# Kernel tuning notes

Measured on AMD Instinct MI355X. Metric: run time of the kernel, lower is better.

The kernel has to match this reference:

```python
import jax, jax.numpy as jnp
import numpy as np

N_NODES = 2048
N_GRAPHS = 64
N_EDGES = 16384
B = 65536
META = 64
TX = 8
NOISE = 128
IN_DIM = N_NODES + 1 + 32 + TX  # 2089


def setup_inputs() -> dict:
    key = jax.random.key(0)
    ks = jax.random.split(key, 11)
    return {
        "batched_graphs": jax.random.randint(ks[0], (B,), 0, N_GRAPHS),
        "batched_chain": jax.random.normal(ks[1], (B,), dtype=jnp.float32),
        "trigger_data": jax.random.normal(ks[2], (B, META), dtype=jnp.float32),
        "tx_start_time": jax.random.normal(ks[3], (B, TX), dtype=jnp.float32),
        "edges": jax.random.randint(ks[4], (N_GRAPHS, 2, N_EDGES), 0, N_NODES),
        "gcn_w": jax.random.normal(ks[5], (), dtype=jnp.float32),
        "gcn_b": jax.random.normal(ks[6], (), dtype=jnp.float32) * 0.01,
        "trig_W": jax.random.normal(ks[7], (META, 32), dtype=jnp.float32) / np.sqrt(META),
        "trig_b": jnp.zeros((32,), dtype=jnp.float32),
        "emb_W": jax.random.normal(ks[8], (IN_DIM, NOISE), dtype=jnp.float32) / np.sqrt(IN_DIM),
        "emb_b": jnp.zeros((NOISE,), dtype=jnp.float32),
    }


def _gcn_one_graph(edge_index, w, b):
    # GCNConv(1,1) on x = ones(n_nodes,1): add self loops, sym-normalize.
    self_idx = jnp.arange(N_NODES, dtype=edge_index.dtype)
    src = jnp.concatenate([edge_index[0], self_idx])
    dst = jnp.concatenate([edge_index[1], self_idx])
    deg = jax.ops.segment_sum(jnp.ones(src.shape[0], jnp.float32), dst,
                              num_segments=N_NODES)
    dinv = jnp.where(deg > 0, jax.lax.rsqrt(deg), 0.0)
    norm = dinv[src] * dinv[dst]
    agg = jax.ops.segment_sum(norm, dst, num_segments=N_NODES)  # [n_nodes]
    return agg * w + b  # x @ W with x==1 is just w per node, plus bias


def reference(batched_graphs, batched_chain, trigger_data, tx_start_time,
              edges, gcn_w, gcn_b, trig_W, trig_b, emb_W, emb_b):
    # Per-graph GCN embeddings for all topologies (covers all uniques). [G, n_nodes]
    graph_emb = jax.vmap(lambda e: _gcn_one_graph(e, gcn_w, gcn_b))(edges)
    ge = graph_emb[batched_graphs]                         # [B, n_nodes] gather
    trig = jax.nn.relu(trigger_data @ trig_W + trig_b)     # [B, 32]
    x = jnp.concatenate(
        [ge, batched_chain[:, None], trig, tx_start_time], axis=1)  # [B, IN_DIM]
    return x @ emb_W + emb_b                               # [B, NOISE]
```

## Files before the change

### kernel.cpp

```cpp
#include <hip/hip_runtime.h>

#define NN 2048
#define NG 64
#define NE 16384
#define BB 65536
#define META 64
#define TXD 8
#define NOISE 128


__global__ __launch_bounds__(256) void agg_kernel(
    const int* __restrict__ edges,
    const float* __restrict__ gcn_w,
    const float* __restrict__ gcn_b,
    float* __restrict__ emb,
    float* __restrict__ graph_out)
{
    __shared__ int                s_cnt[NN];
    __shared__ float              s_dinv[NN];
    __shared__ unsigned long long s_acc[NN];
    const int g = blockIdx.x, tid = threadIdx.x;
    const int4* __restrict__ e4 = (const int4*)(edges + (size_t)g * 2 * NE);

    if (tid < NOISE) graph_out[g * NOISE + tid] = 0.0f;

    int4 ds[16];
    #pragma unroll
    for (int k = 0; k < 16; ++k) ds[k] = e4[4096 + k * 256 + tid];

    for (int n = tid; n < NN; n += 256) { s_cnt[n] = 1; s_acc[n] = 0ull; }
    __syncthreads();

    #pragma unroll
    for (int k = 0; k < 16; ++k) {
        atomicAdd(&s_cnt[ds[k].x], 1);
        atomicAdd(&s_cnt[ds[k].y], 1);
        atomicAdd(&s_cnt[ds[k].z], 1);
        atomicAdd(&s_cnt[ds[k].w], 1);
    }
    __syncthreads();
    for (int n = tid; n < NN; n += 256) s_dinv[n] = rsqrtf((float)s_cnt[n]);
    __syncthreads();

    const float SCALE = 1099511627776.0f;
    #pragma unroll
    for (int k = 0; k < 16; ++k) {
        int4 sr = e4[k * 256 + tid];
        float nx = s_dinv[sr.x] * s_dinv[ds[k].x];
        float ny = s_dinv[sr.y] * s_dinv[ds[k].y];
        float nz = s_dinv[sr.z] * s_dinv[ds[k].z];
        float nw = s_dinv[sr.w] * s_dinv[ds[k].w];
        atomicAdd(&s_acc[ds[k].x], (unsigned long long)(nx * SCALE));
        atomicAdd(&s_acc[ds[k].y], (unsigned long long)(ny * SCALE));
        atomicAdd(&s_acc[ds[k].z], (unsigned long long)(nz * SCALE));
        atomicAdd(&s_acc[ds[k].w], (unsigned long long)(nw * SCALE));
    }
    __syncthreads();

    const float w = gcn_w[0], b = gcn_b[0];
    for (int n = tid; n < NN; n += 256) {
        float di = s_dinv[n];
        float agg = (float)((double)s_acc[n] * 0x1p-40) + di * di;
        emb[(size_t)g * NN + n] = agg * w + b;
    }
}

__global__ __launch_bounds__(256) void fold_kernel(
    const float* __restrict__ emb,
    const float* __restrict__ emb_W,
    float* __restrict__ graph_out)
{
    __shared__ float s_e[128];
    __shared__ float s_red[128];
    const int tid = threadIdx.x;
    const int g = blockIdx.x >> 4, chunk = blockIdx.x & 15;
    const int n0 = chunk * 128;
    if (tid < 128) s_e[tid] = emb[(size_t)g * NN + n0 + tid];
    __syncthreads();
    const int c = tid & 127, h = tid >> 7;
    const float* __restrict__ Wp = emb_W + (size_t)(n0 + h * 64) * NOISE + c;
    const float* __restrict__ ep = s_e + h * 64;
    float a0 = 0.f, a1 = 0.f, a2 = 0.f, a3 = 0.f;
    #pragma unroll
    for (int i = 0; i < 64; i += 4) {
        a0 = fmaf(ep[i + 0], Wp[(i + 0) * NOISE], a0);
        a1 = fmaf(ep[i + 1], Wp[(i + 1) * NOISE], a1);
        a2 = fmaf(ep[i + 2], Wp[(i + 2) * NOISE], a2);
        a3 = fmaf(ep[i + 3], Wp[(i + 3) * NOISE], a3);
    }
    float acc = (a0 + a1) + (a2 + a3);
    if (h == 1) s_red[c] = acc;
    __syncthreads();
    if (h == 0) atomicAdd(&graph_out[g * NOISE + c], acc + s_red[c]);
}

#define ROWS 32
__global__ __launch_bounds__(256) void main_kernel(
    const int* __restrict__ bg,
    const float* __restrict__ chain,
    const float* __restrict__ trig_in,
    const float* __restrict__ txs,
    const float* __restrict__ trig_W,
    const float* __restrict__ trig_b,
    const float* __restrict__ emb_W,
    const float* __restrict__ emb_b,
    const float* __restrict__ graph_out,
    float* __restrict__ out)
{
    __shared__ float s_twT[32 * 68];
    __shared__ float s_tb[32];
    __shared__ float s_td[ROWS * META];
    __shared__ float s_trig[ROWS * 32];
    __shared__ float s_tx[ROWS * TXD];
    __shared__ float s_chain[ROWS];
    __shared__ int   s_g[ROWS];

    const int tid = threadIdx.x;
    const int row0 = blockIdx.x * ROWS;

    for (int k = tid; k < META * 32; k += 256) {
        int i = k >> 5, j = k & 31;
        s_twT[j * 68 + i] = trig_W[k];
    }
    if (tid < 32) s_tb[tid] = trig_b[tid];
    for (int t = tid; t < ROWS * META / 4; t += 256)
        ((float4*)s_td)[t] = ((const float4*)(trig_in + (size_t)row0 * META))[t];
    if (tid < ROWS * TXD / 4)
        ((float4*)s_tx)[tid] = ((const float4*)(txs + (size_t)row0 * TXD))[tid];
    if (tid < ROWS) { s_chain[tid] = chain[row0 + tid]; s_g[tid] = bg[row0 + tid]; }

    const int n = tid & 127;
    float w2[32], w3[TXD];
    #pragma unroll
    for (int j = 0; j < 32; ++j) w2[j] = emb_W[(size_t)(2049 + j) * NOISE + n];
    #pragma unroll
    for (int k = 0; k < TXD; ++k) w3[k] = emb_W[(size_t)(2081 + k) * NOISE + n];
    const float w1 = emb_W[(size_t)2048 * NOISE + n];
    const float bias = emb_b[n];

    __syncthreads();

    {
        const int j = tid & 31, r0 = tid >> 5;
        const float* __restrict__ twj = s_twT + j * 68;
        float acc[4];
        #pragma unroll
        for (int p = 0; p < 4; ++p) acc[p] = s_tb[j];
        #pragma unroll
        for (int i = 0; i < META; i += 4) {
            float4 tw = *(const float4*)(twj + i);
            #pragma unroll
            for (int p = 0; p < 4; ++p) {
                float4 t = *(const float4*)(s_td + (p * 8 + r0) * META + i);
                acc[p] = fmaf(t.x, tw.x, acc[p]);
                acc[p] = fmaf(t.y, tw.y, acc[p]);
                acc[p] = fmaf(t.z, tw.z, acc[p]);
                acc[p] = fmaf(t.w, tw.w, acc[p]);
            }
        }
        #pragma unroll
        for (int p = 0; p < 4; ++p)
            s_trig[(p * 8 + r0) * 32 + j] = fmaxf(acc[p], 0.f);
    }
    __syncthreads();

    const int rb = tid >> 7;
    float go[16], ch[16];
    #pragma unroll
    for (int p = 0; p < 16; ++p) {
        const int r = p * 2 + rb;
        const int g = s_g[r];
        ch[p] = s_chain[r];
        go[p] = graph_out[g * NOISE + n];
    }
    #pragma unroll
    for (int p = 0; p < 16; ++p) {
        const int r = p * 2 + rb;
        const int row = row0 + r;
        float acc = bias + go[p] + ch[p] * w1;
        const float4* __restrict__ tx4 = (const float4*)(s_tx + r * TXD);
        float4 t0 = tx4[0], t1 = tx4[1];
        acc = fmaf(t0.x, w3[0], acc); acc = fmaf(t0.y, w3[1], acc);
        acc = fmaf(t0.z, w3[2], acc); acc = fmaf(t0.w, w3[3], acc);
        acc = fmaf(t1.x, w3[4], acc); acc = fmaf(t1.y, w3[5], acc);
        acc = fmaf(t1.z, w3[6], acc); acc = fmaf(t1.w, w3[7], acc);
        const float4* __restrict__ tg4 = (const float4*)(s_trig + r * 32);
        #pragma unroll
        for (int q = 0; q < 8; ++q) {
            float4 t = tg4[q];
            acc = fmaf(t.x, w2[4 * q + 0], acc);
            acc = fmaf(t.y, w2[4 * q + 1], acc);
            acc = fmaf(t.z, w2[4 * q + 2], acc);
            acc = fmaf(t.w, w2[4 * q + 3], acc);
        }
        out[(size_t)row * NOISE + n] = acc;
    }
}

extern "C" void kernel_launch(void* const* d_in, const int* in_sizes, int n_in,
                              void* d_out, int out_size, void* d_ws, size_t ws_size,
                              hipStream_t stream) {
    const int*   bg      = (const int*)d_in[0];
    const float* chain   = (const float*)d_in[1];
    const float* trig_in = (const float*)d_in[2];
    const float* txs     = (const float*)d_in[3];
    const int*   edges   = (const int*)d_in[4];
    const float* gcn_w   = (const float*)d_in[5];
    const float* gcn_b   = (const float*)d_in[6];
    const float* trig_W  = (const float*)d_in[7];
    const float* trig_b  = (const float*)d_in[8];
    const float* emb_W   = (const float*)d_in[9];
    const float* emb_b   = (const float*)d_in[10];
    float* out = (float*)d_out;

    float* graph_out = (float*)d_ws;
    float* emb       = (float*)d_ws + NG * NOISE;

    agg_kernel<<<NG, 256, 0, stream>>>(edges, gcn_w, gcn_b, emb, graph_out);
    fold_kernel<<<NG * 16, 256, 0, stream>>>(emb, emb_W, graph_out);
    main_kernel<<<BB / ROWS, 256, 0, stream>>>(bg, chain, trig_in, txs, trig_W,
                                               trig_b, emb_W, emb_b, graph_out, out);
}
```

Before: 132.6 us.

## Restructure main kernel with 2x2 register tiling and float2 output columns

Reworks the main kernel so each thread computes a 2x2 tile of the trigger projection, reading padded shared-memory rows to avoid bank conflicts. The output stage now handles two adjacent columns per thread with float2 weights and float2 stores. Per-row scalars (graph index, chain, tx) are read straight from global memory instead of being staged in shared memory. The trig_W transpose uses float4 loads, and launch bounds request three blocks per CU. This doubles the per-thread weight registers, which the occupancy hint may strain.

```diff
diff --git a/kernel.cpp b/kernel.cpp
--- a/kernel.cpp
+++ b/kernel.cpp
@@ -95,7 +95,7 @@
 }
 
 #define ROWS 32
-__global__ __launch_bounds__(256) void main_kernel(
+__global__ __launch_bounds__(256, 3) void main_kernel(
     const int* __restrict__ bg,
     const float* __restrict__ chain,
     const float* __restrict__ trig_in,
@@ -107,93 +107,107 @@
     const float* __restrict__ graph_out,
     float* __restrict__ out)
 {
+    __shared__ float s_td[ROWS * 68];
     __shared__ float s_twT[32 * 68];
-    __shared__ float s_tb[32];
-    __shared__ float s_td[ROWS * META];
-    __shared__ float s_trig[ROWS * 32];
-    __shared__ float s_tx[ROWS * TXD];
-    __shared__ float s_chain[ROWS];
-    __shared__ int   s_g[ROWS];
+    __shared__ float s_trig[ROWS * 36];
 
     const int tid = threadIdx.x;
     const int row0 = blockIdx.x * ROWS;
 
-    for (int k = tid; k < META * 32; k += 256) {
-        int i = k >> 5, j = k & 31;
-        s_twT[j * 68 + i] = trig_W[k];
-    }
-    if (tid < 32) s_tb[tid] = trig_b[tid];
-    for (int t = tid; t < ROWS * META / 4; t += 256)
-        ((float4*)s_td)[t] = ((const float4*)(trig_in + (size_t)row0 * META))[t];
-    if (tid < ROWS * TXD / 4)
-        ((float4*)s_tx)[tid] = ((const float4*)(txs + (size_t)row0 * TXD))[tid];
-    if (tid < ROWS) { s_chain[tid] = chain[row0 + tid]; s_g[tid] = bg[row0 + tid]; }
-
-    const int n = tid & 127;
-    float w2[32], w3[TXD];
-    #pragma unroll
-    for (int j = 0; j < 32; ++j) w2[j] = emb_W[(size_t)(2049 + j) * NOISE + n];
-    #pragma unroll
-    for (int k = 0; k < TXD; ++k) w3[k] = emb_W[(size_t)(2081 + k) * NOISE + n];
-    const float w1 = emb_W[(size_t)2048 * NOISE + n];
-    const float bias = emb_b[n];
-
-    __syncthreads();
-
     {
-        const int j = tid & 31, r0 = tid >> 5;
-        const float* __restrict__ twj = s_twT + j * 68;
-        float acc[4];
-        #pragma unroll
-        for (int p = 0; p < 4; ++p) acc[p] = s_tb[j];
+        const float4* __restrict__ gsrc =
+            (const float4*)(trig_in + (size_t)row0 * META);
+        #pragma unroll
+        for (int k = 0; k < 2; ++k) {
+            int t = tid + k * 256;
+            int r = t >> 4, i4 = t & 15;
+            *(float4*)&s_td[r * 68 + i4 * 4] = gsrc[t];
+        }
+    }
+    {
+        const float4* __restrict__ gsrc = (const float4*)trig_W;
+        #pragma unroll
+        for (int k = 0; k < 2; ++k) {
+            int t = tid + k * 256;
+            int i = t >> 3, j4 = (t & 7) * 4;
+            float4 v = gsrc[t];
+            s_twT[(j4 + 0) * 68 + i] = v.x;
+            s_twT[(j4 + 1) * 68 + i] = v.y;
+            s_twT[(j4 + 2) * 68 + i] = v.z;
+            s_twT[(j4 + 3) * 68 + i] = v.w;
+        }
+    }
+
+    const int n0 = (tid & 63) * 2;
+    float2 w2[32], w3[TXD];
+    #pragma unroll
+    for (int j = 0; j < 32; ++j)
+        w2[j] = *(const float2*)&emb_W[(size_t)(2049 + j) * NOISE + n0];
+    #pragma unroll
+    for (int k = 0; k < TXD; ++k)
+        w3[k] = *(const float2*)&emb_W[(size_t)(2081 + k) * NOISE + n0];
+    const float2 w1   = *(const float2*)&emb_W[(size_t)2048 * NOISE + n0];
+    const float2 bias = *(const float2*)&emb_b[n0];
+
+    __syncthreads();
+
+    {
+        const int j0 = (tid & 15) * 2;
+        const int r0 = (tid >> 4) * 2;
+        const float* __restrict__ tw0 = s_twT + j0 * 68;
+        const float* __restrict__ tw1 = s_twT + (j0 + 1) * 68;
+        const float* __restrict__ td0 = s_td + r0 * 68;
+        const float* __restrict__ td1 = s_td + (r0 + 1) * 68;
+        float b0 = trig_b[j0], b1 = trig_b[j0 + 1];
+        float a00 = b0, a01 = b1, a10 = b0, a11 = b1;
         #pragma unroll
         for (int i = 0; i < META; i += 4) {
-            float4 tw = *(const float4*)(twj + i);
-            #pragma unroll
-            for (int p = 0; p < 4; ++p) {
-                float4 t = *(const float4*)(s_td + (p * 8 + r0) * META + i);
-                acc[p] = fmaf(t.x, tw.x, acc[p]);
-                acc[p] = fmaf(t.y, tw.y, acc[p]);
-                acc[p] = fmaf(t.z, tw.z, acc[p]);
-                acc[p] = fmaf(t.w, tw.w, acc[p]);
-            }
-        }
-        #pragma unroll
-        for (int p = 0; p < 4; ++p)
-            s_trig[(p * 8 + r0) * 32 + j] = fmaxf(acc[p], 0.f);
-    }
-    __syncthreads();
-
-    const int rb = tid >> 7;
-    float go[16], ch[16];
-    #pragma unroll
-    for (int p = 0; p < 16; ++p) {
-        const int r = p * 2 + rb;
-        const int g = s_g[r];
-        ch[p] = s_chain[r];
-        go[p] = graph_out[g * NOISE + n];
-    }
-    #pragma unroll
-    for (int p = 0; p < 16; ++p) {
-        const int r = p * 2 + rb;
+            float4 u0 = *(const float4*)(tw0 + i);
+            float4 u1 = *(const float4*)(tw1 + i);
+            float4 t0 = *(const float4*)(td0 + i);
+            float4 t1 = *(const float4*)(td1 + i);
+            a00 = fmaf(t0.x, u0.x, a00); a00 = fmaf(t0.y, u0.y, a00);
+            a00 = fmaf(t0.z, u0.z, a00); a00 = fmaf(t0.w, u0.w, a00);
+            a01 = fmaf(t0.x, u1.x, a01); a01 = fmaf(t0.y, u1.y, a01);
+            a01 = fmaf(t0.z, u1.z, a01); a01 = fmaf(t0.w, u1.w, a01);
+            a10 = fmaf(t1.x, u0.x, a10); a10 = fmaf(t1.y, u0.y, a10);
+            a10 = fmaf(t1.z, u0.z, a10); a10 = fmaf(t1.w, u0.w, a10);
+            a11 = fmaf(t1.x, u1.x, a11); a11 = fmaf(t1.y, u1.y, a11);
+            a11 = fmaf(t1.z, u1.z, a11); a11 = fmaf(t1.w, u1.w, a11);
+        }
+        s_trig[r0 * 36 + j0]           = fmaxf(a00, 0.f);
+        s_trig[r0 * 36 + j0 + 1]       = fmaxf(a01, 0.f);
+        s_trig[(r0 + 1) * 36 + j0]     = fmaxf(a10, 0.f);
+        s_trig[(r0 + 1) * 36 + j0 + 1] = fmaxf(a11, 0.f);
+    }
+    __syncthreads();
+
+    const int wv = tid >> 6;
+    #pragma unroll
+    for (int p = 0; p < 8; ++p) {
+        const int r = p * 4 + wv;
         const int row = row0 + r;
-        float acc = bias + go[p] + ch[p] * w1;
-        const float4* __restrict__ tx4 = (const float4*)(s_tx + r * TXD);
-        float4 t0 = tx4[0], t1 = tx4[1];
-        acc = fmaf(t0.x, w3[0], acc); acc = fmaf(t0.y, w3[1], acc);
-        acc = fmaf(t0.z, w3[2], acc); acc = fmaf(t0.w, w3[3], acc);
-        acc = fmaf(t1.x, w3[4], acc); acc = fmaf(t1.y, w3[5], acc);
-        acc = fmaf(t1.z, w3[6], acc); acc = fmaf(t1.w, w3[7], acc);
-        const float4* __restrict__ tg4 = (const float4*)(s_trig + r * 32);
+        const int g = bg[row];
+        const float ch = chain[row];
+        const float2 go2 = *(const float2*)&graph_out[g * NOISE + n0];
+        float ax = bias.x + go2.x + ch * w1.x;
+        float ay = bias.y + go2.y + ch * w1.y;
+        #pragma unroll
+        for (int k = 0; k < TXD; ++k) {
+            float t = txs[(size_t)row * TXD + k];
+            ax = fmaf(t, w3[k].x, ax);
+            ay = fmaf(t, w3[k].y, ay);
+        }
+        const float* __restrict__ tg = s_trig + r * 36;
         #pragma unroll
         for (int q = 0; q < 8; ++q) {
-            float4 t = tg4[q];
-            acc = fmaf(t.x, w2[4 * q + 0], acc);
-            acc = fmaf(t.y, w2[4 * q + 1], acc);
-            acc = fmaf(t.z, w2[4 * q + 2], acc);
-            acc = fmaf(t.w, w2[4 * q + 3], acc);
-        }
-        out[(size_t)row * NOISE + n] = acc;
+            float4 t4 = *(const float4*)(tg + q * 4);
+            ax = fmaf(t4.x, w2[4 * q + 0].x, ax); ay = fmaf(t4.x, w2[4 * q + 0].y, ay);
+            ax = fmaf(t4.y, w2[4 * q + 1].x, ax); ay = fmaf(t4.y, w2[4 * q + 1].y, ay);
+            ax = fmaf(t4.z, w2[4 * q + 2].x, ax); ay = fmaf(t4.z, w2[4 * q + 2].y, ay);
+            ax = fmaf(t4.w, w2[4 * q + 3].x, ax); ay = fmaf(t4.w, w2[4 * q + 3].y, ay);
+        }
+        *(float2*)&out[(size_t)row * NOISE + n0] = make_float2(ax, ay);
     }
 }
 
```

Result: no change. 132.4 us (-0.1%).
